# Kernel tuning notes

Measured on AMD Instinct MI355X. Metric: run time of the kernel, lower is better.

Reference implementation:

```python
import math
import jax, jax.numpy as jnp
import numpy as np

NUM_TOKENS = 16384
EMBED_DIM = 256
BATCH = 16
SEQ_N = 1024  # 32x32 latent grid


def setup_inputs() -> dict:
    key = jax.random.key(0)
    k_seq, k_emb = jax.random.split(key)
    seq = jax.random.randint(k_seq, (BATCH, SEQ_N), 0, NUM_TOKENS, dtype=jnp.int64 if jax.config.jax_enable_x64 else jnp.int32)
    embedding = jax.random.normal(k_emb, (NUM_TOKENS, EMBED_DIM), dtype=jnp.float32)
    return {"seq": seq, "embedding": embedding}


def reference(seq, embedding):
    # Faithful to the source: one_hot(seq) @ embedding.weight.
    # (Mathematically identical to embedding[seq]; this is the pattern with
    # kernel headroom.)
    num_tokens = embedding.shape[0]
    one_hot = jax.nn.one_hot(seq, num_tokens, dtype=embedding.dtype)  # [b, n, K]
    embed = jnp.einsum('bnk,kd->bnd', one_hot, embedding)             # [b, n, d]
    b, n, d = embed.shape
    h = w = int(math.isqrt(n))  # n is static under jit
    # view(b, h, w, d).permute(0, 3, 1, 2) -> NCHW
    return embed.reshape(b, h, w, d).transpose(0, 3, 1, 2)
```

## Files before the change

kernel.cpp:

```cpp
#include <hip/hip_runtime.h>

#define BATCH       16
#define SEQ_N       1024
#define EMBED_DIM   256
#define NTILE       16
#define LDS_STRIDE4 65

typedef float f32x4 __attribute__((ext_vector_type(4)));

__global__ __launch_bounds__(512) void
embed_gather_transpose(const int* __restrict__ seq,
                       const float* __restrict__ emb,
                       float* __restrict__ out) {
    __shared__ f32x4 lds4[NTILE * LDS_STRIDE4];
    const float* lds = reinterpret_cast<const float*>(lds4);

    const int b  = blockIdx.x >> 6;
    const int n0 = (blockIdx.x & 63) << 4;
    const int* seqb = seq + b * SEQ_N + n0;

#pragma unroll
    for (int i = 0; i < 2; ++i) {
        const int flat = i * 512 + threadIdx.x;
        const int nn   = flat >> 6;
        const int c4   = flat & 63;
        const int row  = seqb[nn];
        lds4[nn * LDS_STRIDE4 + c4] =
            reinterpret_cast<const f32x4*>(emb + (size_t)row * EMBED_DIM)[c4];
    }
    __syncthreads();

    float* outb = out + ((size_t)b * EMBED_DIM) * SEQ_N + n0;
#pragma unroll
    for (int i = 0; i < 2; ++i) {
        const int flat = i * 512 + threadIdx.x;
        const int d    = flat >> 2;
        const int q    = flat & 3;
        const int nn   = q << 2;
        f32x4 v;
        v.x = lds[(nn + 0) * (LDS_STRIDE4 * 4) + d];
        v.y = lds[(nn + 1) * (LDS_STRIDE4 * 4) + d];
        v.z = lds[(nn + 2) * (LDS_STRIDE4 * 4) + d];
        v.w = lds[(nn + 3) * (LDS_STRIDE4 * 4) + d];
        reinterpret_cast<f32x4*>(outb + (size_t)d * SEQ_N)[q] = v;
    }
}

extern "C" void kernel_launch(void* const* d_in, const int* in_sizes, int n_in,
                              void* d_out, int out_size, void* d_ws, size_t ws_size,
                              hipStream_t stream) {
    const int*   seq = (const int*)d_in[0];
    const float* emb = (const float*)d_in[1];
    float*       out = (float*)d_out;

    const int grid = BATCH * (SEQ_N / NTILE);
    embed_gather_transpose<<<grid, 512, 0, stream>>>(seq, emb, out);
}
```

Measured before the change: 11.91 us.

## Replace LDS-staged transpose with direct per-lane gather and nontemporal column stores

Drops the shared-memory staging tile and barrier. Each lane now owns one sequence position and loads 16 contiguous embedding floats as four 16-byte vectors, then writes them to 16 output rows. Each store across a wave covers 64 consecutive n, which keeps stores coalesced at 256 bytes per row. The gather loads become strided across lanes (one random row each) rather than fully contiguous per row. Nontemporal stores are added to avoid polluting the cache with output data.

```diff
diff --git a/kernel.cpp b/kernel.cpp
--- a/kernel.cpp
+++ b/kernel.cpp
@@ -1,49 +1,51 @@
 #include <hip/hip_runtime.h>
 
-#define BATCH       16
-#define SEQ_N       1024
-#define EMBED_DIM   256
-#define NTILE       16
-#define LDS_STRIDE4 65
+#define BATCH     16
+#define SEQ_N     1024
+#define EMBED_DIM 256
 
 typedef float f32x4 __attribute__((ext_vector_type(4)));
 
-__global__ __launch_bounds__(512) void
-embed_gather_transpose(const int* __restrict__ seq,
-                       const float* __restrict__ emb,
-                       float* __restrict__ out) {
-    __shared__ f32x4 lds4[NTILE * LDS_STRIDE4];
-    const float* lds = reinterpret_cast<const float*>(lds4);
+__global__ __launch_bounds__(256) void
+embed_gather_direct(const int* __restrict__ seq,
+                    const float* __restrict__ emb,
+                    float* __restrict__ out) {
+    const int wave = threadIdx.x >> 6;
+    const int lane = threadIdx.x & 63;
 
-    const int b  = blockIdx.x >> 6;
-    const int n0 = (blockIdx.x & 63) << 4;
-    const int* seqb = seq + b * SEQ_N + n0;
+    const int dgroup = blockIdx.x & 3;
+    const int nchunk = (blockIdx.x >> 2) & 15;
+    const int b      = blockIdx.x >> 6;
 
-#pragma unroll
-    for (int i = 0; i < 2; ++i) {
-        const int flat = i * 512 + threadIdx.x;
-        const int nn   = flat >> 6;
-        const int c4   = flat & 63;
-        const int row  = seqb[nn];
-        lds4[nn * LDS_STRIDE4 + c4] =
-            reinterpret_cast<const f32x4*>(emb + (size_t)row * EMBED_DIM)[c4];
-    }
-    __syncthreads();
+    const int n  = (nchunk << 6) + lane;
+    const int d0 = (dgroup << 6) + (wave << 4);
 
-    float* outb = out + ((size_t)b * EMBED_DIM) * SEQ_N + n0;
-#pragma unroll
-    for (int i = 0; i < 2; ++i) {
-        const int flat = i * 512 + threadIdx.x;
-        const int d    = flat >> 2;
-        const int q    = flat & 3;
-        const int nn   = q << 2;
-        f32x4 v;
-        v.x = lds[(nn + 0) * (LDS_STRIDE4 * 4) + d];
-        v.y = lds[(nn + 1) * (LDS_STRIDE4 * 4) + d];
-        v.z = lds[(nn + 2) * (LDS_STRIDE4 * 4) + d];
-        v.w = lds[(nn + 3) * (LDS_STRIDE4 * 4) + d];
-        reinterpret_cast<f32x4*>(outb + (size_t)d * SEQ_N)[q] = v;
-    }
+    const int row = seq[b * SEQ_N + n];
+
+    const f32x4* src =
+        reinterpret_cast<const f32x4*>(emb + (size_t)row * EMBED_DIM + d0);
+    const f32x4 v0 = src[0];
+    const f32x4 v1 = src[1];
+    const f32x4 v2 = src[2];
+    const f32x4 v3 = src[3];
+
+    float* o = out + ((size_t)b * EMBED_DIM + d0) * SEQ_N + n;
+    __builtin_nontemporal_store(v0.x, o + 0  * SEQ_N);
+    __builtin_nontemporal_store(v0.y, o + 1  * SEQ_N);
+    __builtin_nontemporal_store(v0.z, o + 2  * SEQ_N);
+    __builtin_nontemporal_store(v0.w, o + 3  * SEQ_N);
+    __builtin_nontemporal_store(v1.x, o + 4  * SEQ_N);
+    __builtin_nontemporal_store(v1.y, o + 5  * SEQ_N);
+    __builtin_nontemporal_store(v1.z, o + 6  * SEQ_N);
+    __builtin_nontemporal_store(v1.w, o + 7  * SEQ_N);
+    __builtin_nontemporal_store(v2.x, o + 8  * SEQ_N);
+    __builtin_nontemporal_store(v2.y, o + 9  * SEQ_N);
+    __builtin_nontemporal_store(v2.z, o + 10 * SEQ_N);
+    __builtin_nontemporal_store(v2.w, o + 11 * SEQ_N);
+    __builtin_nontemporal_store(v3.x, o + 12 * SEQ_N);
+    __builtin_nontemporal_store(v3.y, o + 13 * SEQ_N);
+    __builtin_nontemporal_store(v3.z, o + 14 * SEQ_N);
+    __builtin_nontemporal_store(v3.w, o + 15 * SEQ_N);
 }
 
 extern "C" void kernel_launch(void* const* d_in, const int* in_sizes, int n_in,
@@ -53,6 +55,6 @@
     const float* emb = (const float*)d_in[1];
     float*       out = (float*)d_out;
 
-    const int grid = BATCH * (SEQ_N / NTILE);
-    embed_gather_transpose<<<grid, 512, 0, stream>>>(seq, emb, out);
+    const int grid = BATCH * (SEQ_N / 64) * (EMBED_DIM / 64);
+    embed_gather_direct<<<grid, 256, 0, stream>>>(seq, emb, out);
 }
```

Result: slower. 16.32 us (+37.1%).
